# Kernel optimization log

Measured on AMD Instinct MI355X. Metric: run time of the kernel, lower is better.

Reference implementation:

```python
import jax, jax.numpy as jnp
import numpy as np

KNN_K = 5          # neighbor count hard-coded in the original forward (get_entropy(..., k=5))
SAMPLE_K = 256     # self.k: number of tokens sampled per batch item
EPS = 1e-12


def _knn_entropy(x):
    """Per-point k-NN entropy weight: distance to the KNN_K-th nearest neighbor.

    x: [B, N, D] -> [B, N] nonnegative weights (Kozachenko-Leonenko style; the
    per-point entropy contribution is monotone in log d_k, and multinomial
    weights must be nonnegative, so we use d_k itself as the weight).
    """
    B, N, D = x.shape
    sq = jnp.sum(x * x, axis=-1)                                   # [B, N]
    d2 = sq[:, :, None] + sq[:, None, :] - 2.0 * jnp.einsum('bnd,bmd->bnm', x, x)  # [B,N,N]
    d2 = jnp.maximum(d2, 0.0)
    idx = jnp.arange(N)
    d2 = d2.at[:, idx, idx].set(jnp.inf)                           # exclude self
    neg_smallest, _ = jax.lax.top_k(-d2, KNN_K)                    # [B, N, KNN_K]
    dk2 = -neg_smallest[..., -1]                                   # sq dist to k-th NN
    return jnp.sqrt(dk2 + EPS)                                     # [B, N]


def setup_inputs() -> dict:
    key = jax.random.key(0)
    x = jax.random.normal(key, (8, 4096, 256), dtype=jnp.float32)
    return {"x": x}


def reference(x):
    # entropy weights per token (batched; replaces the per-batch numpy loop)
    w = _knn_entropy(x)                                            # [B, N]
    # multinomial sampling WITHOUT replacement via Gumbel top-k trick
    key = jax.random.key(42)
    g = jax.random.gumbel(key, w.shape, dtype=w.dtype)             # [B, N]
    scores = jnp.log(w + EPS) + g
    _, sampled_idx = jax.lax.top_k(scores, SAMPLE_K)               # [B, SAMPLE_K]
    # gather sampled tokens
    sampled = jnp.take_along_axis(x, sampled_idx[:, :, None], axis=1)  # [B, SAMPLE_K, D]
    return (sampled, 0.0)
```

## Files before the change

kernel.cpp:

```cpp
#include <hip/hip_runtime.h>
#include <math.h>
#include <stdint.h>

#define BATCH 8
#define NTOK  4096
#define DIM   256
#define SK    256
#define BQ    128
#define BM    128
#define BK    128
#define MH    2048
#define TOPK  10
#define CANDH 44

typedef __attribute__((ext_vector_type(8))) _Float16 half8;
typedef __attribute__((ext_vector_type(4))) float float4v;
typedef __attribute__((ext_vector_type(16))) float f32x16;

#define GLOAD_LDS16(gp, lp)                                                    \
  __builtin_amdgcn_global_load_lds(                                            \
      (const __attribute__((address_space(1))) unsigned int*)(gp),             \
      (__attribute__((address_space(3))) unsigned int*)(lp), 16, 0, 0)

__device__ __forceinline__ uint32_t umin32(uint32_t a, uint32_t b) { return a < b ? a : b; }
__device__ __forceinline__ uint32_t umax32(uint32_t a, uint32_t b) { return a > b ? a : b; }

__device__ __forceinline__ uint32_t rotl32(uint32_t v, uint32_t r) {
  return (v << r) | (v >> (32u - r));
}
__device__ __forceinline__ void tf_round4(uint32_t& x0, uint32_t& x1,
                                          uint32_t r0, uint32_t r1,
                                          uint32_t r2, uint32_t r3) {
  x0 += x1; x1 = rotl32(x1, r0); x1 ^= x0;
  x0 += x1; x1 = rotl32(x1, r1); x1 ^= x0;
  x0 += x1; x1 = rotl32(x1, r2); x1 ^= x0;
  x0 += x1; x1 = rotl32(x1, r3); x1 ^= x0;
}
__device__ __forceinline__ uint32_t threefry_bits32(uint32_t c_hi, uint32_t c_lo) {
  const uint32_t k0 = 0u, k1 = 42u;
  const uint32_t k2 = k0 ^ k1 ^ 0x1BD11BDAu;
  uint32_t x0 = c_hi + k0;
  uint32_t x1 = c_lo + k1;
  tf_round4(x0, x1, 13u, 15u, 26u, 6u);  x0 += k1; x1 += k2 + 1u;
  tf_round4(x0, x1, 17u, 29u, 16u, 24u); x0 += k2; x1 += k0 + 2u;
  tf_round4(x0, x1, 13u, 15u, 26u, 6u);  x0 += k0; x1 += k1 + 3u;
  tf_round4(x0, x1, 17u, 29u, 16u, 24u); x0 += k1; x1 += k2 + 4u;
  tf_round4(x0, x1, 13u, 15u, 26u, 6u);  x0 += k2; x1 += k0 + 5u;
  return x0 ^ x1;
}

__global__ __launch_bounds__(256) void tofp16_rowsq_kernel(
    const float* __restrict__ x, unsigned short* __restrict__ xh,
    float* __restrict__ sqf) {
  const int row  = blockIdx.x * 4 + (threadIdx.x >> 6);
  const int lane = threadIdx.x & 63;
  const float* xr = x + (size_t)row * DIM;
  double acc = 0.0;
#pragma unroll
  for (int i = 0; i < 4; ++i) {
    const float v = xr[lane + i * 64];
    const _Float16 h = (_Float16)v;
    xh[(size_t)row * DIM + lane + i * 64] = *(const unsigned short*)&h;
    acc += (double)v * (double)v;
  }
#pragma unroll
  for (int off = 32; off > 0; off >>= 1) acc += __shfl_down(acc, off, 64);
  if (lane == 0) sqf[row] = (float)acc;
}

__global__ __launch_bounds__(256, 2) void gemm_knn_kernel(
    const unsigned short* __restrict__ xh, const float* __restrict__ sqf,
    int* __restrict__ cand) {
  __shared__ union {
    unsigned short Bf[2][16384];
    uint32_t M[512][10];
  } U;

  const int wid = (blockIdx.x & 7) * 64 + (blockIdx.x >> 3);
  const int b   = wid >> 6;
  const int qt  = (wid >> 1) & 31;
  const int mh  = wid & 1;
  const int q0  = qt * BQ;
  const int mbase = mh * MH;
  const int t  = threadIdx.x;
  const int w  = t >> 6;
  const int l  = t & 63;
  const int l5 = l & 31;
  const int hi2 = l >> 5;

  const unsigned short* xhb = xh + (size_t)b * NTOK * DIM;
  const float* sqb = sqf + b * NTOK;

  auto stageB = [&](int buf, int m0s, int kb) {
    const int m = m0s + w * 32 + l5;
    const unsigned short* src = xhb + (size_t)m * DIM + kb + hi2 * 8;
#pragma unroll
    for (int c = 0; c < 8; ++c) {
      GLOAD_LDS16(src + c * 16,
                  (char*)&U.Bf[0][0] + buf * 32768 + (c * 4 + w) * 1024 + l * 16);
    }
  };
  stageB(0, mbase, 0);

  const int qg = q0 + w * 32 + l5;
  const unsigned short* qrow = xhb + (size_t)qg * DIM;
  half8 af[16];
#pragma unroll
  for (int kk = 0; kk < 16; ++kk)
    af[kk] = *(const half8*)(qrow + kk * 16 + hi2 * 8);
  const float sqq = sqb[qg];

  __syncthreads();

  uint32_t tv0[TOPK], tv1[TOPK];
#pragma unroll
  for (int j = 0; j < TOPK; ++j) { tv0[j] = 0xFFFFFFFFu; tv1[j] = 0xFFFFFFFFu; }

  for (int mt = 0; mt < MH / BM; ++mt) {
    const int m0 = mbase + mt * BM;
    f32x16 acc[4];
#pragma unroll
    for (int ii = 0; ii < 4; ++ii) acc[ii] = (f32x16)(0.0f);

#pragma unroll
    for (int ks2 = 0; ks2 < 2; ++ks2) {
      const int s = mt * 2 + ks2;
      const int buf = s & 1;
      if (s + 1 < (MH / BM) * 2) {
        const int sn = s + 1;
        stageB(buf ^ 1, mbase + (sn >> 1) * BM, (sn & 1) * BK);
      }
#pragma unroll
      for (int kap = 0; kap < 8; ++kap) {
        const int kk = ks2 * 8 + kap;
#pragma unroll
        for (int ii = 0; ii < 4; ++ii) {
          const half8 mf = *(const half8*)((const char*)&U.Bf[0][0] +
                                           buf * 32768 + (kap * 4 + ii) * 1024 + l * 16);
          acc[ii] = __builtin_amdgcn_mfma_f32_32x32x16_f16(mf, af[kk], acc[ii], 0, 0, 0);
        }
      }
      __syncthreads();
    }

#pragma unroll
    for (int ii = 0; ii < 4; ++ii) {
      const int mb = m0 + ii * 32 + hi2 * 4;
#pragma unroll
      for (int c = 0; c < 4; ++c) {
        const float4v sqm = *(const float4v*)(sqb + mb + c * 8);
        uint32_t* tv = (c < 2) ? tv0 : tv1;
#pragma unroll
        for (int r = 0; r < 4; ++r) {
          const int mg = mb + c * 8 + r;
          const float d2a = fmaxf(sqq + sqm[r] - 2.0f * acc[ii][c * 4 + r], 0.0f);
          uint32_t u = (__float_as_uint(d2a) & 0xFFFFF000u) | (uint32_t)mg;
          u = (mg == qg) ? 0xFFFFFFFFu : u;
          if (u < tv[TOPK - 1]) {
            uint32_t v = u;
#pragma unroll
            for (int k2 = 0; k2 < TOPK; ++k2) {
              const uint32_t lo = umin32(tv[k2], v);
              v = umax32(tv[k2], v);
              tv[k2] = lo;
            }
          }
        }
      }
    }
  }

  __syncthreads();
  {
    const int base = ((w * 32 + l5) << 2) + (hi2 << 1);
#pragma unroll
    for (int j = 0; j < TOPK; ++j) { U.M[base][j] = tv0[j]; U.M[base + 1][j] = tv1[j]; }
  }
  __syncthreads();
  if (t < BQ) {
    const int q = t;
    uint32_t t5[5] = {0xFFFFFFFFu, 0xFFFFFFFFu, 0xFFFFFFFFu, 0xFFFFFFFFu, 0xFFFFFFFFu};
    for (int s = 0; s < 4; ++s)
      for (int j = 0; j < 5; ++j) {
        const uint32_t v = U.M[q * 4 + s][j];
        if (v < t5[4]) {
          uint32_t vv = v;
#pragma unroll
          for (int k2 = 0; k2 < 5; ++k2) {
            const uint32_t lo = umin32(t5[k2], vv);
            vv = umax32(t5[k2], vv);
            t5[k2] = lo;
          }
        }
      }
    const float T = __uint_as_float(t5[4] & 0xFFFFF000u) + 2.0f;
    int cnt = 0, ov = 0;
    int* cq = cand + (size_t)(b * NTOK + q0 + q) * (2 * CANDH) + mh * CANDH;
    for (int s = 0; s < 4; ++s) {
      const uint32_t last = U.M[q * 4 + s][TOPK - 1];
      if (__uint_as_float(last & 0xFFFFF000u) < T) ov = 1;
      for (int j = 0; j < TOPK; ++j) {
        const uint32_t v = U.M[q * 4 + s][j];
        if (__uint_as_float(v & 0xFFFFF000u) <= T && cnt < 4 * TOPK)
          cq[1 + cnt++] = (int)(v & 0xFFFu);
      }
    }
    cq[0] = ov ? -1 : cnt;
  }
}

__global__ __launch_bounds__(256) void exact_knn_score_kernel(
    const float* __restrict__ x, const int* __restrict__ cand,
    double* __restrict__ scores) {
  const int qg = blockIdx.x * 4 + (threadIdx.x >> 6);
  const int l  = threadIdx.x & 63;
  const int b  = qg >> 12;
  const int q  = qg & (NTOK - 1);
  const float* xb = x + (size_t)b * NTOK * DIM;
  const int* cq = cand + (size_t)qg * (2 * CANDH);

  double xq[4];
#pragma unroll
  for (int i = 0; i < 4; ++i) xq[i] = (double)xb[(size_t)q * DIM + l + i * 64];

  double t5[5] = {1e300, 1e300, 1e300, 1e300, 1e300};
  auto process = [&](int m) {
    double acc = 0.0;
#pragma unroll
    for (int i = 0; i < 4; ++i) {
      const double d = xq[i] - (double)xb[(size_t)m * DIM + l + i * 64];
      acc += d * d;
    }
#pragma unroll
    for (int off = 32; off > 0; off >>= 1) acc += __shfl_xor(acc, off, 64);
    if (acc < t5[4]) {
      t5[4] = acc;
#pragma unroll
      for (int k2 = 4; k2 > 0; --k2)
        if (t5[k2] < t5[k2 - 1]) { double tmp = t5[k2]; t5[k2] = t5[k2 - 1]; t5[k2 - 1] = tmp; }
    }
  };

  for (int h = 0; h < 2; ++h) {
    const int cnt = cq[h * CANDH];
    if (cnt >= 0) {
      for (int c = 0; c < cnt; ++c) process(cq[h * CANDH + 1 + c]);
    } else {
      const int mb = h * MH;
      for (int m = mb; m < mb + MH; ++m) {
        if (m == q) continue;
        process(m);
      }
    }
  }

  if (l == 0) {
    const uint32_t bits = threefry_bits32(0u, (uint32_t)qg);
    const uint32_t fb = (bits >> 9) | 0x3F800000u;
    float uf = __uint_as_float(fb) - 1.0f;
    const float tiny = 1.17549435082228750797e-38f;
    uf += tiny;
    if (uf < tiny) uf = tiny;
    const double g = -log(-log((double)uf));
    const double wv = sqrt(t5[4] + 1e-12);
    scores[qg] = log(wv + 1e-12) + g;
  }
}

__global__ __launch_bounds__(1024) void sort_topk_kernel(
    const double* __restrict__ scores, int* __restrict__ sel) {
  __shared__ unsigned long long ko[NTOK];
  __shared__ int ki[NTOK];
  const int b = blockIdx.x;
  const int t = threadIdx.x;
  for (int i = t; i < NTOK; i += 1024) {
    const double s = scores[(size_t)b * NTOK + i];
    unsigned long long u = (unsigned long long)__double_as_longlong(s);
    u = (u & 0x8000000000000000ull) ? ~u : (u | 0x8000000000000000ull);
    ko[i] = u; ki[i] = i;
  }
  __syncthreads();
  for (int k = 2; k <= NTOK; k <<= 1) {
    for (int j = k >> 1; j > 0; j >>= 1) {
      for (int base = 0; base < NTOK; base += 1024) {
        const int i = base + t;
        const int p = i ^ j;
        if (p > i) {
          const bool up = (i & k) == 0;
          unsigned long long a = ko[i], c = ko[p];
          int ia = ki[i], ic = ki[p];
          const bool p_beats = (c > a) || (c == a && ic < ia);
          const bool i_beats = (a > c) || (a == c && ia < ic);
          const bool sw = up ? p_beats : i_beats;
          if (sw) { ko[i] = c; ko[p] = a; ki[i] = ic; ki[p] = ia; }
        }
      }
      __syncthreads();
    }
  }
  if (t < SK) sel[b * SK + t] = ki[t];
}

__global__ __launch_bounds__(256) void gather_kernel(const float* __restrict__ x,
                                                     const int* __restrict__ sel,
                                                     float* __restrict__ out) {
  const int blk = blockIdx.x;
  const int b = blk >> 8;
  const int r = blk & 255;
  const int t = threadIdx.x;
  const int src = sel[b * SK + r];
  out[((size_t)(b * SK + r)) * DIM + t] = x[((size_t)(b * NTOK + src)) * DIM + t];
  if (blk == 0 && t == 0) out[(size_t)BATCH * SK * DIM] = 0.0f;
}

extern "C" void kernel_launch(void* const* d_in, const int* in_sizes, int n_in,
                              void* d_out, int out_size, void* d_ws, size_t ws_size,
                              hipStream_t stream) {
  const float* x = (const float*)d_in[0];
  float* out = (float*)d_out;
  char* ws = (char*)d_ws;

  double* scores  = (double*)(ws + 0);
  float*  sqf     = (float*)(ws + 262144);
  int*    sel     = (int*)(ws + 393216);
  unsigned short* xh = (unsigned short*)(ws + 1048576);
  int*    cand    = (int*)(ws + 17825792);

  tofp16_rowsq_kernel<<<BATCH * NTOK / 4, 256, 0, stream>>>(x, xh, sqf);
  gemm_knn_kernel<<<BATCH * (NTOK / BQ) * 2, 256, 0, stream>>>(xh, sqf, cand);
  exact_knn_score_kernel<<<BATCH * NTOK / 4, 256, 0, stream>>>(x, cand, scores);
  sort_topk_kernel<<<BATCH, 1024, 0, stream>>>(scores, sel);
  gather_kernel<<<BATCH * SK, 256, 0, stream>>>(x, sel, out);
}
```

Measured before the change: 454.3 us.

## Halve K-tile staging to shrink LDS and drop per-element self-exclusion from GEMM epilogue

Cuts the K-slice staged per step from 128 to 64, which halves the LDS double buffer and doubles the number of pipeline steps. The aim is lower LDS usage, which may allow more resident blocks or finer-grained overlap. It also removes the clamp and self-index masking from the hot top-k epilogue. To compensate, the merge keeps the 6 smallest candidates and picks the threshold index based on whether the query lies in this half, and the exact rescoring pass now skips the self index. The cost is more barriers per tile, and negative distances from rounding can now reach the candidate lists.

```diff
diff --git a/kernel.cpp b/kernel.cpp
--- a/kernel.cpp
+++ b/kernel.cpp
@@ -8,7 +8,7 @@
 #define SK    256
 #define BQ    128
 #define BM    128
-#define BK    128
+#define BK    64
 #define MH    2048
 #define TOPK  10
 #define CANDH 44
@@ -72,7 +72,7 @@
     const unsigned short* __restrict__ xh, const float* __restrict__ sqf,
     int* __restrict__ cand) {
   __shared__ union {
-    unsigned short Bf[2][16384];
+    unsigned short Bf[2][8192];
     uint32_t M[512][10];
   } U;
 
@@ -95,9 +95,9 @@
     const int m = m0s + w * 32 + l5;
     const unsigned short* src = xhb + (size_t)m * DIM + kb + hi2 * 8;
 #pragma unroll
-    for (int c = 0; c < 8; ++c) {
+    for (int c = 0; c < 4; ++c) {
       GLOAD_LDS16(src + c * 16,
-                  (char*)&U.Bf[0][0] + buf * 32768 + (c * 4 + w) * 1024 + l * 16);
+                  (char*)&U.Bf[0][0] + buf * 16384 + (c * 4 + w) * 1024 + l * 16);
     }
   };
   stageB(0, mbase, 0);
@@ -123,20 +123,20 @@
     for (int ii = 0; ii < 4; ++ii) acc[ii] = (f32x16)(0.0f);
 
 #pragma unroll
-    for (int ks2 = 0; ks2 < 2; ++ks2) {
-      const int s = mt * 2 + ks2;
+    for (int ks = 0; ks < 4; ++ks) {
+      const int s = mt * 4 + ks;
       const int buf = s & 1;
-      if (s + 1 < (MH / BM) * 2) {
+      if (s + 1 < (MH / BM) * 4) {
         const int sn = s + 1;
-        stageB(buf ^ 1, mbase + (sn >> 1) * BM, (sn & 1) * BK);
-      }
-#pragma unroll
-      for (int kap = 0; kap < 8; ++kap) {
-        const int kk = ks2 * 8 + kap;
+        stageB(buf ^ 1, mbase + (sn >> 2) * BM, (sn & 3) * BK);
+      }
+#pragma unroll
+      for (int kap = 0; kap < 4; ++kap) {
+        const int kk = ks * 4 + kap;
 #pragma unroll
         for (int ii = 0; ii < 4; ++ii) {
           const half8 mf = *(const half8*)((const char*)&U.Bf[0][0] +
-                                           buf * 32768 + (kap * 4 + ii) * 1024 + l * 16);
+                                           buf * 16384 + (kap * 4 + ii) * 1024 + l * 16);
           acc[ii] = __builtin_amdgcn_mfma_f32_32x32x16_f16(mf, af[kk], acc[ii], 0, 0, 0);
         }
       }
@@ -153,9 +153,8 @@
 #pragma unroll
         for (int r = 0; r < 4; ++r) {
           const int mg = mb + c * 8 + r;
-          const float d2a = fmaxf(sqq + sqm[r] - 2.0f * acc[ii][c * 4 + r], 0.0f);
-          uint32_t u = (__float_as_uint(d2a) & 0xFFFFF000u) | (uint32_t)mg;
-          u = (mg == qg) ? 0xFFFFFFFFu : u;
+          const float d2a = sqq + sqm[r] - 2.0f * acc[ii][c * 4 + r];
+          const uint32_t u = (__float_as_uint(d2a) & 0xFFFFF000u) | (uint32_t)mg;
           if (u < tv[TOPK - 1]) {
             uint32_t v = u;
 #pragma unroll
@@ -179,23 +178,27 @@
   __syncthreads();
   if (t < BQ) {
     const int q = t;
-    uint32_t t5[5] = {0xFFFFFFFFu, 0xFFFFFFFFu, 0xFFFFFFFFu, 0xFFFFFFFFu, 0xFFFFFFFFu};
+    const int qglob = q0 + q;
+    const int kidx = ((qglob >> 11) == mh) ? 5 : 4;
+    uint32_t t6[6];
+#pragma unroll
+    for (int j = 0; j < 6; ++j) t6[j] = 0xFFFFFFFFu;
     for (int s = 0; s < 4; ++s)
-      for (int j = 0; j < 5; ++j) {
+      for (int j = 0; j < 6; ++j) {
         const uint32_t v = U.M[q * 4 + s][j];
-        if (v < t5[4]) {
+        if (v < t6[5]) {
           uint32_t vv = v;
 #pragma unroll
-          for (int k2 = 0; k2 < 5; ++k2) {
-            const uint32_t lo = umin32(t5[k2], vv);
-            vv = umax32(t5[k2], vv);
-            t5[k2] = lo;
+          for (int k2 = 0; k2 < 6; ++k2) {
+            const uint32_t lo = umin32(t6[k2], vv);
+            vv = umax32(t6[k2], vv);
+            t6[k2] = lo;
           }
         }
       }
-    const float T = __uint_as_float(t5[4] & 0xFFFFF000u) + 2.0f;
+    const float T = __uint_as_float(t6[kidx] & 0xFFFFF000u) + 2.0f;
     int cnt = 0, ov = 0;
-    int* cq = cand + (size_t)(b * NTOK + q0 + q) * (2 * CANDH) + mh * CANDH;
+    int* cq = cand + (size_t)(b * NTOK + qglob) * (2 * CANDH) + mh * CANDH;
     for (int s = 0; s < 4; ++s) {
       const uint32_t last = U.M[q * 4 + s][TOPK - 1];
       if (__uint_as_float(last & 0xFFFFF000u) < T) ov = 1;
@@ -244,7 +247,11 @@
   for (int h = 0; h < 2; ++h) {
     const int cnt = cq[h * CANDH];
     if (cnt >= 0) {
-      for (int c = 0; c < cnt; ++c) process(cq[h * CANDH + 1 + c]);
+      for (int c = 0; c < cnt; ++c) {
+        const int m = cq[h * CANDH + 1 + c];
+        if (m == q) continue;
+        process(m);
+      }
     } else {
       const int mb = h * MH;
       for (int m = mb; m < mb + MH; ++m) {
```

After: 448.3 us. Within noise of the previous version (-1.3%).
